# Performance work log

Hardware: AMD Instinct MI355X
Metric: run time of the kernel (lower is better)

Reference implementation:

```python
import jax, jax.numpy as jnp
import numpy as np

QLEN, BSZ, DM, NH, DH, FF = 1024, 4, 512, 8, 64, 2048
EPS = 1e-5


def layer_norm(x, g, b):
    mu = x.mean(-1, keepdims=True)
    var = ((x - mu) ** 2).mean(-1, keepdims=True)
    return (x - mu) / jnp.sqrt(var + EPS) * g + b


def rel_pos_emb(qlen, klen, d_model, bsz):
    # XLNet-style 'bi' relative positional encoding: positions klen .. -qlen+1
    freq = jnp.arange(0, d_model, 2, dtype=jnp.float32)
    inv_freq = 1.0 / (10000.0 ** (freq / d_model))
    pos_seq = jnp.arange(klen, -qlen, -1, dtype=jnp.float32)  # [klen+qlen]
    sinusoid = pos_seq[:, None] * inv_freq[None, :]           # [klen+qlen, d/2]
    pe = jnp.concatenate([jnp.sin(sinusoid), jnp.cos(sinusoid)], -1)
    return jnp.broadcast_to(pe[:, None, :], (pe.shape[0], bsz, d_model))


def rel_shift(x, klen):
    # x: [q, p, b, n] with p = klen + qlen
    q, p, b, n = x.shape
    x = x.reshape(p, q, b, n)[1:]
    x = x.reshape(q, p - 1, b, n)[:, :klen]
    return x


def setup_inputs() -> dict:
    key = jax.random.key(0)
    ks = jax.random.split(key, 20)
    s = 0.02
    inp = {
        'src': jax.random.normal(ks[0], (QLEN, BSZ, DM), jnp.float32),
        'q_w': jax.random.normal(ks[1], (DM, NH, DH), jnp.float32) * s,
        'k_w': jax.random.normal(ks[2], (DM, NH, DH), jnp.float32) * s,
        'v_w': jax.random.normal(ks[3], (DM, NH, DH), jnp.float32) * s,
        'r_w': jax.random.normal(ks[4], (DM, NH, DH), jnp.float32) * s,
        'o_w': jax.random.normal(ks[5], (DM, NH, DH), jnp.float32) * s,
        'r_w_bias': jax.random.normal(ks[6], (NH, DH), jnp.float32) * s,
        'r_r_bias': jax.random.normal(ks[7], (NH, DH), jnp.float32) * s,
        'w1': jax.random.normal(ks[8], (FF, DM), jnp.float32) * s,
        'b1': jnp.zeros((FF,), jnp.float32),
        'w2': jax.random.normal(ks[9], (DM, FF), jnp.float32) * s,
        'b2': jnp.zeros((DM,), jnp.float32),
        'g1': jnp.ones((DM,), jnp.float32), 'be1': jnp.zeros((DM,), jnp.float32),
        'g2': jnp.ones((DM,), jnp.float32), 'be2': jnp.zeros((DM,), jnp.float32),
        'gf': jnp.ones((DM,), jnp.float32), 'bf': jnp.zeros((DM,), jnp.float32),
        'src_mask': jnp.triu(jnp.ones((QLEN, QLEN), bool), k=1),
    }
    return inp


def reference(src, q_w, k_w, v_w, r_w, o_w, r_w_bias, r_r_bias,
              w1, b1, w2, b2, g1, be1, g2, be2, gf, bf, src_mask):
    qlen, bsz, dm = src.shape
    klen = qlen  # mems=None
    scale = 1.0 / (DH ** 0.5)
    pos_emb = rel_pos_emb(qlen, klen, dm, bsz)  # [klen+qlen, b, d]
    mask = src_mask.astype(src.dtype)

    # --- RelativeMultiheadAttention (single weight-shared encoder layer) ---
    cat = src  # no memory
    q_head = jnp.einsum('ibh,hnd->ibnd', src, q_w)
    k_head = jnp.einsum('ibh,hnd->ibnd', cat, k_w)
    v_head = jnp.einsum('ibh,hnd->ibnd', cat, v_w)
    k_pos = jnp.einsum('ibh,hnd->ibnd', pos_emb, r_w)

    ac = jnp.einsum('ibnd,jbnd->ijbn', q_head + r_w_bias, k_head)
    bd = jnp.einsum('ibnd,jbnd->ijbn', q_head + r_r_bias, k_pos)
    bd = rel_shift(bd, klen)

    score = (ac + bd) * scale - 1e30 * mask[:, :, None, None]
    prob = jax.nn.softmax(score, axis=1)
    attn_vec = jnp.einsum('ijbn,jbnd->ibnd', prob, v_head)
    attn_out = jnp.einsum('ibnd,hnd->ibh', attn_vec, o_w)

    x = layer_norm(src + attn_out, g1, be1)
    ffn = jax.nn.gelu(x @ w1.T + b1, approximate=False) @ w2.T + b2
    x = layer_norm(x + ffn, g2, be2)

    # final encoder norm
    out = layer_norm(x, gf, bf)
    return out
```

## Files before the change

kernel.cpp:

```cpp
#include <hip/hip_runtime.h>

#define QLEN 1024
#define BSZ  4
#define DM   512
#define NH   8
#define DH   64
#define FFD  2048

static constexpr float LN_EPS = 1e-5f;

typedef __attribute__((ext_vector_type(8))) short short8_t;
typedef __attribute__((ext_vector_type(4))) float f32x4;

__device__ __forceinline__ ushort f2b(float f) {
  uint u = __float_as_uint(f);
  return (ushort)((u + 0x7FFFu + ((u >> 16) & 1u)) >> 16);
}
__device__ __forceinline__ float b2f(ushort h) {
  return __uint_as_float(((uint)h) << 16);
}

__device__ __forceinline__ void cvt8_body(const float* in, ushort* out, int idx) {
  const float4 f0 = *reinterpret_cast<const float4*>(in + (size_t)idx * 8);
  const float4 f1 = *reinterpret_cast<const float4*>(in + (size_t)idx * 8 + 4);
  uint p0 = f2b(f0.x) | ((uint)f2b(f0.y) << 16);
  uint p1 = f2b(f0.z) | ((uint)f2b(f0.w) << 16);
  uint p2 = f2b(f1.x) | ((uint)f2b(f1.y) << 16);
  uint p3 = f2b(f1.z) | ((uint)f2b(f1.w) << 16);
  int4 st; st.x = (int)p0; st.y = (int)p1; st.z = (int)p2; st.w = (int)p3;
  *reinterpret_cast<int4*>(out + (size_t)idx * 8) = st;
}

__global__ __launch_bounds__(256) void prep_kernel(
    const float* __restrict__ src, const float* __restrict__ o_w,
    const float* __restrict__ w1, const float* __restrict__ w2,
    const float* __restrict__ qw, const float* __restrict__ kw,
    const float* __restrict__ vw, const float* __restrict__ rw,
    ushort* __restrict__ peb, ushort* __restrict__ srcb,
    ushort* __restrict__ owb, ushort* __restrict__ w1b,
    ushort* __restrict__ w2b, ushort* __restrict__ qkvw,
    ushort* __restrict__ rwT) {
  __shared__ float tile[32][33];
  const int bid = blockIdx.x, t = threadIdx.x;
  if (bid < 2048) {
    const int idx = bid * 256 + t;
    const int r = idx >> 9, f = idx & 511, f0 = f & 255;
    float invf = __expf(-(float)f0 * (9.210340371976184f / 256.0f));
    float arg  = (float)r * invf;
    peb[idx] = f2b((f < 256) ? __sinf(arg) : __cosf(arg));
  } else if (bid < 3072) {
    cvt8_body(src, srcb, (bid - 2048) * 256 + t);
  } else if (bid < 3200) {
    cvt8_body(o_w, owb, (bid - 3072) * 256 + t);
  } else if (bid < 3712) {
    cvt8_body(w1, w1b, (bid - 3200) * 256 + t);
  } else if (bid < 4224) {
    cvt8_body(w2, w2b, (bid - 3712) * 256 + t);
  } else {
    const int e = bid - 4224;
    const int z = e >> 8, rem = e & 255, bx = rem & 15, by = rem >> 4;
    const float* in = (z == 0) ? qw : (z == 1) ? kw : (z == 2) ? vw : rw;
    const int nd0 = bx * 32, h0 = by * 32;
    const int tx = t & 31, ty = t >> 5;
#pragma unroll
    for (int k = 0; k < 4; ++k)
      tile[ty + 8 * k][tx] = in[(size_t)(h0 + ty + 8 * k) * 512 + nd0 + tx];
    __syncthreads();
    ushort* out = (z < 3) ? (qkvw + (size_t)z * 512 * 512) : rwT;
#pragma unroll
    for (int k = 0; k < 4; ++k)
      out[(size_t)(nd0 + ty + 8 * k) * 512 + h0 + tx] = f2b(tile[tx][ty + 8 * k]);
  }
}

template <int EPI>
__global__ __launch_bounds__(256) void gemm_bf16(
    const ushort* __restrict__ A, const ushort* __restrict__ B,
    const float* __restrict__ bias, void* __restrict__ Cout,
    int M, int N, int K) {
  __shared__ ushort As[64 * 40];
  __shared__ ushort Bs[128 * 40];
  const int t = threadIdx.x;
  const int w = t >> 6, l = t & 63;
  const int lc = l & 15, lq = l >> 4;
  const int bm = blockIdx.y * 64, bn = blockIdx.x * 128;
  const int wr = (w >> 1) * 32, wc = (w & 1) * 64;
  const int sr = t >> 2, sk = (t & 3) * 8;

  f32x4 acc[2][4];
#pragma unroll
  for (int i = 0; i < 2; ++i)
#pragma unroll
    for (int j = 0; j < 4; ++j) acc[i][j] = (f32x4){0.f, 0.f, 0.f, 0.f};

  int4 a_v = *reinterpret_cast<const int4*>(A + (size_t)(bm + sr) * K + sk);
  int4 b0v = *reinterpret_cast<const int4*>(B + (size_t)(bn + sr) * K + sk);
  int4 b1v = *reinterpret_cast<const int4*>(B + (size_t)(bn + 64 + sr) * K + sk);

  for (int k0 = 0; k0 < K; k0 += 32) {
    *reinterpret_cast<int4*>(As + sr * 40 + sk) = a_v;
    *reinterpret_cast<int4*>(Bs + sr * 40 + sk) = b0v;
    *reinterpret_cast<int4*>(Bs + (64 + sr) * 40 + sk) = b1v;
    __syncthreads();
    if (k0 + 32 < K) {
      a_v = *reinterpret_cast<const int4*>(A + (size_t)(bm + sr) * K + k0 + 32 + sk);
      b0v = *reinterpret_cast<const int4*>(B + (size_t)(bn + sr) * K + k0 + 32 + sk);
      b1v = *reinterpret_cast<const int4*>(B + (size_t)(bn + 64 + sr) * K + k0 + 32 + sk);
    }
    short8_t af[2], bf[4];
#pragma unroll
    for (int mf = 0; mf < 2; ++mf)
      af[mf] = *reinterpret_cast<const short8_t*>(As + (wr + mf * 16 + lc) * 40 + lq * 8);
#pragma unroll
    for (int nf = 0; nf < 4; ++nf)
      bf[nf] = *reinterpret_cast<const short8_t*>(Bs + (wc + nf * 16 + lc) * 40 + lq * 8);
#pragma unroll
    for (int mf = 0; mf < 2; ++mf)
#pragma unroll
      for (int nf = 0; nf < 4; ++nf)
        acc[mf][nf] = __builtin_amdgcn_mfma_f32_16x16x32_bf16(af[mf], bf[nf], acc[mf][nf], 0, 0, 0);
    __syncthreads();
  }

#pragma unroll
  for (int mf = 0; mf < 2; ++mf)
#pragma unroll
    for (int nf = 0; nf < 4; ++nf) {
      const int col = bn + wc + nf * 16 + lc;
#pragma unroll
      for (int reg = 0; reg < 4; ++reg) {
        const int row = bm + wr + mf * 16 + lq * 4 + reg;
        float v = acc[mf][nf][reg];
        if (EPI == 2 || EPI == 3) v += bias[col];
        if (EPI == 2) v = 0.5f * v * (1.0f + erff(v * 0.70710678118654752f));
        if (EPI == 0 || EPI == 2)
          ((ushort*)Cout)[(size_t)row * N + col] = f2b(v);
        else
          ((float*)Cout)[(size_t)row * N + col] = v;
      }
    }
}

template <int EPI>
__global__ __launch_bounds__(256) void gemm128(
    const ushort* __restrict__ A, const ushort* __restrict__ B,
    const float* __restrict__ bias, void* __restrict__ Cout,
    int M, int N, int K) {
  __shared__ ushort As[128 * 40];
  __shared__ ushort Bs[128 * 40];
  const int t = threadIdx.x;
  const int w = t >> 6, l = t & 63;
  const int lc = l & 15, lq = l >> 4;
  const int bm = blockIdx.y * 128, bn = blockIdx.x * 128;
  const int wr = (w >> 1) * 64, wc = (w & 1) * 64;
  const int sr = t >> 2, sk = (t & 3) * 8;

  f32x4 acc[4][4];
#pragma unroll
  for (int i = 0; i < 4; ++i)
#pragma unroll
    for (int j = 0; j < 4; ++j) acc[i][j] = (f32x4){0.f, 0.f, 0.f, 0.f};

  int4 a0v = *reinterpret_cast<const int4*>(A + (size_t)(bm + sr) * K + sk);
  int4 a1v = *reinterpret_cast<const int4*>(A + (size_t)(bm + 64 + sr) * K + sk);
  int4 b0v = *reinterpret_cast<const int4*>(B + (size_t)(bn + sr) * K + sk);
  int4 b1v = *reinterpret_cast<const int4*>(B + (size_t)(bn + 64 + sr) * K + sk);

  for (int k0 = 0; k0 < K; k0 += 32) {
    *reinterpret_cast<int4*>(As + sr * 40 + sk) = a0v;
    *reinterpret_cast<int4*>(As + (64 + sr) * 40 + sk) = a1v;
    *reinterpret_cast<int4*>(Bs + sr * 40 + sk) = b0v;
    *reinterpret_cast<int4*>(Bs + (64 + sr) * 40 + sk) = b1v;
    __syncthreads();
    if (k0 + 32 < K) {
      a0v = *reinterpret_cast<const int4*>(A + (size_t)(bm + sr) * K + k0 + 32 + sk);
      a1v = *reinterpret_cast<const int4*>(A + (size_t)(bm + 64 + sr) * K + k0 + 32 + sk);
      b0v = *reinterpret_cast<const int4*>(B + (size_t)(bn + sr) * K + k0 + 32 + sk);
      b1v = *reinterpret_cast<const int4*>(B + (size_t)(bn + 64 + sr) * K + k0 + 32 + sk);
    }
    short8_t af[4], bf[4];
#pragma unroll
    for (int mf = 0; mf < 4; ++mf)
      af[mf] = *reinterpret_cast<const short8_t*>(As + (wr + mf * 16 + lc) * 40 + lq * 8);
#pragma unroll
    for (int nf = 0; nf < 4; ++nf)
      bf[nf] = *reinterpret_cast<const short8_t*>(Bs + (wc + nf * 16 + lc) * 40 + lq * 8);
#pragma unroll
    for (int mf = 0; mf < 4; ++mf)
#pragma unroll
      for (int nf = 0; nf < 4; ++nf)
        acc[mf][nf] = __builtin_amdgcn_mfma_f32_16x16x32_bf16(af[mf], bf[nf], acc[mf][nf], 0, 0, 0);
    __syncthreads();
  }

#pragma unroll
  for (int mf = 0; mf < 4; ++mf)
#pragma unroll
    for (int nf = 0; nf < 4; ++nf) {
      const int col = bn + wc + nf * 16 + lc;
#pragma unroll
      for (int reg = 0; reg < 4; ++reg) {
        const int row = bm + wr + mf * 16 + lq * 4 + reg;
        float v = acc[mf][nf][reg];
        if (EPI == 2 || EPI == 3) v += bias[col];
        if (EPI == 2) v = 0.5f * v * (1.0f + erff(v * 0.70710678118654752f));
        if (EPI == 0 || EPI == 2)
          ((ushort*)Cout)[(size_t)row * N + col] = f2b(v);
        else
          ((float*)Cout)[(size_t)row * N + col] = v;
      }
    }
}

__global__ __launch_bounds__(256) void gemm_split(
    const ushort* __restrict__ A, const ushort* __restrict__ B,
    float* __restrict__ Cout, int M, int N, int K, int halfK) {
  __shared__ ushort As[64 * 40];
  __shared__ ushort Bs[128 * 40];
  const int t = threadIdx.x;
  const int w = t >> 6, l = t & 63;
  const int lc = l & 15, lq = l >> 4;
  const int bm = blockIdx.y * 64, bn = blockIdx.x * 128;
  const int wr = (w >> 1) * 32, wc = (w & 1) * 64;
  const int sr = t >> 2, sk = (t & 3) * 8;
  const int kbeg = blockIdx.z * halfK, kend = kbeg + halfK;
  float* C = Cout + (size_t)blockIdx.z * M * N;

  f32x4 acc[2][4];
#pragma unroll
  for (int i = 0; i < 2; ++i)
#pragma unroll
    for (int j = 0; j < 4; ++j) acc[i][j] = (f32x4){0.f, 0.f, 0.f, 0.f};

  int4 a_v = *reinterpret_cast<const int4*>(A + (size_t)(bm + sr) * K + kbeg + sk);
  int4 b0v = *reinterpret_cast<const int4*>(B + (size_t)(bn + sr) * K + kbeg + sk);
  int4 b1v = *reinterpret_cast<const int4*>(B + (size_t)(bn + 64 + sr) * K + kbeg + sk);

  for (int k0 = kbeg; k0 < kend; k0 += 32) {
    *reinterpret_cast<int4*>(As + sr * 40 + sk) = a_v;
    *reinterpret_cast<int4*>(Bs + sr * 40 + sk) = b0v;
    *reinterpret_cast<int4*>(Bs + (64 + sr) * 40 + sk) = b1v;
    __syncthreads();
    if (k0 + 32 < kend) {
      a_v = *reinterpret_cast<const int4*>(A + (size_t)(bm + sr) * K + k0 + 32 + sk);
      b0v = *reinterpret_cast<const int4*>(B + (size_t)(bn + sr) * K + k0 + 32 + sk);
      b1v = *reinterpret_cast<const int4*>(B + (size_t)(bn + 64 + sr) * K + k0 + 32 + sk);
    }
    short8_t af[2], bf[4];
#pragma unroll
    for (int mf = 0; mf < 2; ++mf)
      af[mf] = *reinterpret_cast<const short8_t*>(As + (wr + mf * 16 + lc) * 40 + lq * 8);
#pragma unroll
    for (int nf = 0; nf < 4; ++nf)
      bf[nf] = *reinterpret_cast<const short8_t*>(Bs + (wc + nf * 16 + lc) * 40 + lq * 8);
#pragma unroll
    for (int mf = 0; mf < 2; ++mf)
#pragma unroll
      for (int nf = 0; nf < 4; ++nf)
        acc[mf][nf] = __builtin_amdgcn_mfma_f32_16x16x32_bf16(af[mf], bf[nf], acc[mf][nf], 0, 0, 0);
    __syncthreads();
  }

#pragma unroll
  for (int mf = 0; mf < 2; ++mf)
#pragma unroll
    for (int nf = 0; nf < 4; ++nf) {
      const int col = bn + wc + nf * 16 + lc;
#pragma unroll
      for (int reg = 0; reg < 4; ++reg) {
        const int row = bm + wr + mf * 16 + lq * 4 + reg;
        C[(size_t)row * N + col] = acc[mf][nf][reg];
      }
    }
}

__global__ __launch_bounds__(256) void repack_kernel(
    const ushort* __restrict__ qkv, const float* __restrict__ rwb,
    const float* __restrict__ rrb, ushort* __restrict__ qaF,
    ushort* __restrict__ qbF, ushort* __restrict__ kF, ushort* __restrict__ vF) {
  __shared__ ushort st[32][72];
  const int t = threadIdx.x, l = t & 63, lc = l & 15, lq = l >> 4;
  const int tile = blockIdx.x, head = blockIdx.y, role = blockIdx.z;
  const int b = head >> 3, n = head & 7;
  const int s0 = tile * 32;
  const int sec = (role == 0) ? 0 : (role == 1) ? 512 : 1024;
  {
    const int s = t >> 3, d8 = (t & 7) * 8;
    int4 rd = *reinterpret_cast<const int4*>(
        qkv + (size_t)((s0 + s) * 4 + b) * 1536 + sec + n * 64 + d8);
    *reinterpret_cast<int4*>(&st[s][d8]) = rd;
  }
  __syncthreads();
  if (role == 0) {
    const int f = t >> 6, sub = f >> 1, kc = f & 1;
    const int row = sub * 16 + lc, k = kc * 32 + lq * 8;
    short8_t qv = *reinterpret_cast<const short8_t*>(&st[row][k]);
    const float4 w0 = *reinterpret_cast<const float4*>(rwb + n * 64 + k);
    const float4 w1 = *reinterpret_cast<const float4*>(rwb + n * 64 + k + 4);
    const float4 u0 = *reinterpret_cast<const float4*>(rrb + n * 64 + k);
    const float4 u1 = *reinterpret_cast<const float4*>(rrb + n * 64 + k + 4);
    const float wv[8] = {w0.x, w0.y, w0.z, w0.w, w1.x, w1.y, w1.z, w1.w};
    const float uv[8] = {u0.x, u0.y, u0.z, u0.w, u1.x, u1.y, u1.z, u1.w};
    short8_t a_, b_;
#pragma unroll
    for (int e = 0; e < 8; ++e) {
      float q = b2f((ushort)qv[e]);
      a_[e] = (short)f2b(q + wv[e]);
      b_[e] = (short)f2b(q + uv[e]);
    }
    const size_t o = ((size_t)((head * 64 + tile * 2 + sub) * 2 + kc)) * 512 + l * 8;
    *reinterpret_cast<short8_t*>(qaF + o) = a_;
    *reinterpret_cast<short8_t*>(qbF + o) = b_;
  } else if (role == 1) {
    const int f = t >> 6, sub = f >> 1, kc = f & 1;
    const int row = sub * 16 + lc, k = kc * 32 + lq * 8;
    short8_t kv = *reinterpret_cast<const short8_t*>(&st[row][k]);
    const size_t o = ((size_t)((head * 64 + tile * 2 + sub) * 2 + kc)) * 512 + l * 8;
    *reinterpret_cast<short8_t*>(kF + o) = kv;
  } else {
    const int nf = t >> 6;
    short8_t vv;
#pragma unroll
    for (int e = 0; e < 8; ++e) vv[e] = (short)st[lq * 8 + e][nf * 16 + lc];
    const size_t o = ((size_t)((head * 32 + tile) * 4 + nf)) * 512 + l * 8;
    *reinterpret_cast<short8_t*>(vF + o) = vv;
  }
}

__global__ __launch_bounds__(128) void kprelF_kernel(
    const ushort* __restrict__ kprel, ushort* __restrict__ kprelF) {
  const int t = threadIdx.x, l = t & 63, lc = l & 15, lq = l >> 4;
  const int kc = t >> 6;
  const int m = blockIdx.x, n = blockIdx.y;
  const int rho = m * 16 - 31 + lc;
  short8_t v;
  if (rho >= 0 && rho < 1024)
    v = *reinterpret_cast<const short8_t*>(kprel + (size_t)rho * 512 + n * 64 + kc * 32 + lq * 8);
  else
#pragma unroll
    for (int e = 0; e < 8; ++e) v[e] = 0;
  const size_t o = ((size_t)((n * 66 + m) * 2 + kc)) * 512 + l * 8;
  *reinterpret_cast<short8_t*>(kprelF + o) = v;
}

__global__ __launch_bounds__(256, 4) void attn_mfma(
    const ushort* __restrict__ qaF, const ushort* __restrict__ qbF,
    const ushort* __restrict__ kF, const ushort* __restrict__ kpF,
    const ushort* __restrict__ vF, ushort* __restrict__ av) {
  __shared__ __align__(16) char smemU[22016];

  const int t = threadIdx.x, w = t >> 6, l = t & 63;
  const int lid = blockIdx.y * 32 + blockIdx.x;
  const int head = (lid & 7) * 4 + ((lid >> 3) & 3);
  const int pr   = lid >> 5;
  const int b = head >> 3, n = head & 7;
  const int lc = l & 15, lq = l >> 4;

  float*  gw = reinterpret_cast<float*>(smemU) + w * (16 * 66);
  ushort* pw = reinterpret_cast<ushort*>(smemU + 16896) + w * (16 * 40);

  for (int ph = 0; ph < 2; ++ph) {
    const int it = ph ? 63 - pr : pr;
    const int i0 = it * 16;
    __syncthreads();

    short8_t qa[2], qb[2];
    {
      const size_t qo = ((size_t)(head * 64 + it) * 2) * 512 + l * 8;
      qa[0] = *reinterpret_cast<const short8_t*>(qaF + qo);
      qa[1] = *reinterpret_cast<const short8_t*>(qaF + qo + 512);
      qb[0] = *reinterpret_cast<const short8_t*>(qbF + qo);
      qb[1] = *reinterpret_cast<const short8_t*>(qbF + qo + 512);
    }

    float m_run[4], l_lane[4];
    f32x4 oacc[4];
#pragma unroll
    for (int reg = 0; reg < 4; ++reg) { m_run[reg] = -1e30f; l_lane[reg] = 0.f; }
#pragma unroll
    for (int nf = 0; nf < 4; ++nf) oacc[nf] = (f32x4){0.f, 0.f, 0.f, 0.f};

    const int nj = it / 2 + 1;

    for (int jt = w; jt < nj; jt += 4) {
      const int j0 = jt * 32;
      const int D = i0 - j0;

      f32x4 sacc[2];
#pragma unroll
      for (int nf = 0; nf < 2; ++nf) sacc[nf] = (f32x4){0.f, 0.f, 0.f, 0.f};
#pragma unroll
      for (int kc = 0; kc < 2; ++kc)
#pragma unroll
        for (int nf = 0; nf < 2; ++nf) {
          short8_t kf = *reinterpret_cast<const short8_t*>(
              kF + ((size_t)((head * 64 + (j0 >> 4) + nf) * 2 + kc)) * 512 + l * 8);
          sacc[nf] = __builtin_amdgcn_mfma_f32_16x16x32_bf16(qa[kc], kf, sacc[nf], 0, 0, 0);
        }

      f32x4 gacc[3];
#pragma unroll
      for (int nf = 0; nf < 3; ++nf) gacc[nf] = (f32x4){0.f, 0.f, 0.f, 0.f};
#pragma unroll
      for (int kc = 0; kc < 2; ++kc)
#pragma unroll
        for (int nf = 0; nf < 3; ++nf) {
          short8_t pf = *reinterpret_cast<const short8_t*>(
              kpF + ((size_t)((n * 66 + (D >> 4) + nf) * 2 + kc)) * 512 + l * 8);
          gacc[nf] = __builtin_amdgcn_mfma_f32_16x16x32_bf16(qb[kc], pf, gacc[nf], 0, 0, 0);
        }

#pragma unroll
      for (int nf = 0; nf < 3; ++nf)
#pragma unroll
        for (int reg = 0; reg < 4; ++reg)
          gw[(lq * 4 + reg) * 66 + nf * 16 + lc] = gacc[nf][reg];

      float s0v[4], s1v[4];
#pragma unroll
      for (int reg = 0; reg < 4; ++reg) {
        const int r = lq * 4 + reg;
        const int c0 = lc, c1 = 16 + lc;
        float s0 = (sacc[0][reg] + gw[r * 66 + (r - c0 + 31)]) * 0.125f;
        float s1 = (sacc[1][reg] + gw[r * 66 + (r - c1 + 31)]) * 0.125f;
        if (D < 32) {
          if (c0 > D + r) s0 = -1e30f;
          if (c1 > D + r) s1 = -1e30f;
        }
        s0v[reg] = s0; s1v[reg] = s1;
      }
      bool ok = true;
#pragma unroll
      for (int reg = 0; reg < 4; ++reg)
        ok &= (fmaxf(s0v[reg], s1v[reg]) <= m_run[reg] + 8.0f);
      if (__all(ok ? 1 : 0)) {
#pragma unroll
        for (int reg = 0; reg < 4; ++reg) {
          const int r = lq * 4 + reg;
          const float p0 = __expf(s0v[reg] - m_run[reg]);
          const float p1 = __expf(s1v[reg] - m_run[reg]);
          l_lane[reg] += p0 + p1;
          pw[r * 40 + lc] = f2b(p0);
          pw[r * 40 + 16 + lc] = f2b(p1);
        }
      } else {
#pragma unroll
        for (int reg = 0; reg < 4; ++reg) {
          const int r = lq * 4 + reg;
          float tm = fmaxf(s0v[reg], s1v[reg]);
          tm = fmaxf(tm, __shfl_xor(tm, 1));
          tm = fmaxf(tm, __shfl_xor(tm, 2));
          tm = fmaxf(tm, __shfl_xor(tm, 4));
          tm = fmaxf(tm, __shfl_xor(tm, 8));
          const float mn = fmaxf(m_run[reg], tm);
          const float corr = __expf(m_run[reg] - mn);
          const float p0 = __expf(s0v[reg] - mn), p1 = __expf(s1v[reg] - mn);
          l_lane[reg] = l_lane[reg] * corr + (p0 + p1);
          m_run[reg] = mn;
#pragma unroll
          for (int nf = 0; nf < 4; ++nf) oacc[nf][reg] *= corr;
          pw[r * 40 + lc] = f2b(p0);
          pw[r * 40 + 16 + lc] = f2b(p1);
        }
      }

      short8_t pa = *reinterpret_cast<const short8_t*>(pw + lc * 40 + lq * 8);
#pragma unroll
      for (int nf = 0; nf < 4; ++nf) {
        short8_t vf = *reinterpret_cast<const short8_t*>(
            vF + ((size_t)((head * 32 + jt) * 4 + nf)) * 512 + l * 8);
        oacc[nf] = __builtin_amdgcn_mfma_f32_16x16x32_bf16(pa, vf, oacc[nf], 0, 0, 0);
      }
    }

    float l_run[4];
#pragma unroll
    for (int reg = 0; reg < 4; ++reg) {
      float v = l_lane[reg];
      v += __shfl_xor(v, 1);
      v += __shfl_xor(v, 2);
      v += __shfl_xor(v, 4);
      v += __shfl_xor(v, 8);
      l_run[reg] = v;
    }

    __syncthreads();
    float* obuf = reinterpret_cast<float*>(smemU);
    float* mlb  = reinterpret_cast<float*>(smemU + 4352);

    if (lc == 0) {
#pragma unroll
      for (int reg = 0; reg < 4; ++reg) {
        const int r = lq * 4 + reg;
        mlb[(w * 16 + r) * 2 + 0] = m_run[reg];
        mlb[(w * 16 + r) * 2 + 1] = l_run[reg];
      }
    }
    for (int i = t; i < 16 * 68; i += 256) obuf[i] = 0.f;
    __syncthreads();

    float scl[4];
#pragma unroll
    for (int reg = 0; reg < 4; ++reg) {
      const int r = lq * 4 + reg;
      const float m0 = mlb[r * 2], m1 = mlb[(16 + r) * 2],
                  m2 = mlb[(32 + r) * 2], m3 = mlb[(48 + r) * 2];
      const float ms = fmaxf(fmaxf(m0, m1), fmaxf(m2, m3));
      scl[reg] = __expf(mlb[(w * 16 + r) * 2] - ms);
    }
#pragma unroll
    for (int ww = 0; ww < 4; ++ww) {
      if (w == ww) {
#pragma unroll
        for (int nf = 0; nf < 4; ++nf)
#pragma unroll
          for (int reg = 0; reg < 4; ++reg) {
            const int r = lq * 4 + reg;
            obuf[r * 68 + nf * 16 + lc] += scl[reg] * oacc[nf][reg];
          }
      }
      __syncthreads();
    }

    {
      const int r = t >> 4, d0 = (t & 15) * 4;
      const float m0 = mlb[r * 2], m1 = mlb[(16 + r) * 2],
                  m2 = mlb[(32 + r) * 2], m3 = mlb[(48 + r) * 2];
      const float ms = fmaxf(fmaxf(m0, m1), fmaxf(m2, m3));
      const float ls = mlb[r * 2 + 1] * __expf(m0 - ms) + mlb[(16 + r) * 2 + 1] * __expf(m1 - ms) +
                       mlb[(32 + r) * 2 + 1] * __expf(m2 - ms) + mlb[(48 + r) * 2 + 1] * __expf(m3 - ms);
      const float inv = 1.f / ls;
      uint pk0 = (uint)f2b(obuf[r * 68 + d0] * inv) | ((uint)f2b(obuf[r * 68 + d0 + 1] * inv) << 16);
      uint pk1 = (uint)f2b(obuf[r * 68 + d0 + 2] * inv) | ((uint)f2b(obuf[r * 68 + d0 + 3] * inv) << 16);
      int2 st2; st2.x = (int)pk0; st2.y = (int)pk1;
      const int tok = (i0 + r) * 4 + b;
      *reinterpret_cast<int2*>(av + (size_t)tok * 512 + n * 64 + d0) = st2;
    }
  }
}

__device__ __forceinline__ float blk_sum(float v, volatile float* sb) {
  v += __shfl_xor(v, 1);  v += __shfl_xor(v, 2);  v += __shfl_xor(v, 4);
  v += __shfl_xor(v, 8);  v += __shfl_xor(v, 16); v += __shfl_xor(v, 32);
  const int t = threadIdx.x;
  if ((t & 63) == 0) sb[t >> 6] = v;
  __syncthreads();
  v = sb[0] + sb[1] + sb[2] + sb[3];
  __syncthreads();
  return v;
}

__global__ __launch_bounds__(256) void ln_res_kernel(
    const float* __restrict__ aoa, const float* __restrict__ aob,
    const float* __restrict__ res,
    const float* __restrict__ g, const float* __restrict__ be,
    float* __restrict__ out, ushort* __restrict__ outb) {
  __shared__ float sb[4];
  const int row = blockIdx.x, t = threadIdx.x;
  const size_t base = (size_t)row * DM;
  const float x0 = aoa[base + t] + aob[base + t] + res[base + t];
  const float x1 = aoa[base + t + 256] + aob[base + t + 256] + res[base + t + 256];
  const float mu = blk_sum(x0 + x1, sb) * (1.f / DM);
  const float d0 = x0 - mu, d1 = x1 - mu;
  const float var = blk_sum(d0 * d0 + d1 * d1, sb) * (1.f / DM);
  const float inv = rsqrtf(var + LN_EPS);
  const float z0 = d0 * inv * g[t] + be[t];
  const float z1 = d1 * inv * g[t + 256] + be[t + 256];
  out[base + t] = z0;
  out[base + t + 256] = z1;
  outb[base + t] = f2b(z0);
  outb[base + t + 256] = f2b(z1);
}

__global__ __launch_bounds__(256) void ln_final_kernel(
    const float* __restrict__ ya, const float* __restrict__ yb,
    const float* __restrict__ b2, const float* __restrict__ xres,
    const float* __restrict__ g2, const float* __restrict__ be2,
    const float* __restrict__ gf, const float* __restrict__ bf,
    float* __restrict__ out) {
  __shared__ float sb[4];
  const int row = blockIdx.x, t = threadIdx.x;
  const size_t base = (size_t)row * DM;
  const float x0 = ya[base + t] + yb[base + t] + b2[t] + xres[base + t];
  const float x1 = ya[base + t + 256] + yb[base + t + 256] + b2[t + 256] + xres[base + t + 256];
  const float mu = blk_sum(x0 + x1, sb) * (1.f / DM);
  const float d0 = x0 - mu, d1 = x1 - mu;
  const float var = blk_sum(d0 * d0 + d1 * d1, sb) * (1.f / DM);
  const float inv = rsqrtf(var + LN_EPS);
  const float z0 = d0 * inv * g2[t] + be2[t];
  const float z1 = d1 * inv * g2[t + 256] + be2[t + 256];
  const float mu2 = blk_sum(z0 + z1, sb) * (1.f / DM);
  const float e0 = z0 - mu2, e1 = z1 - mu2;
  const float var2 = blk_sum(e0 * e0 + e1 * e1, sb) * (1.f / DM);
  const float inv2 = rsqrtf(var2 + LN_EPS);
  out[base + t]       = e0 * inv2 * gf[t] + bf[t];
  out[base + t + 256] = e1 * inv2 * gf[t + 256] + bf[t + 256];
}

extern "C" void kernel_launch(void* const* d_in, const int* in_sizes, int n_in,
                              void* d_out, int out_size, void* d_ws, size_t ws_size,
                              hipStream_t stream) {
  const float* src = (const float*)d_in[0];
  const float* q_w = (const float*)d_in[1];
  const float* k_w = (const float*)d_in[2];
  const float* v_w = (const float*)d_in[3];
  const float* r_w = (const float*)d_in[4];
  const float* o_w = (const float*)d_in[5];
  const float* rwb = (const float*)d_in[6];
  const float* rrb = (const float*)d_in[7];
  const float* w1  = (const float*)d_in[8];
  const float* b1  = (const float*)d_in[9];
  const float* w2  = (const float*)d_in[10];
  const float* b2  = (const float*)d_in[11];
  const float* g1  = (const float*)d_in[12];
  const float* be1 = (const float*)d_in[13];
  const float* g2  = (const float*)d_in[14];
  const float* be2 = (const float*)d_in[15];
  const float* gf  = (const float*)d_in[16];
  const float* bf  = (const float*)d_in[17];

  char* ws = (char*)d_ws;
  const size_t KB = 1024, MB = 1024 * 1024;
  ushort* srcb   = (ushort*)(ws);
  ushort* qkvw   = (ushort*)(ws + 4 * MB);
  ushort* rwT    = (ushort*)(ws + 5 * MB + 512 * KB);
  ushort* owb    = (ushort*)(ws + 6 * MB);
  ushort* w1b    = (ushort*)(ws + 6 * MB + 512 * KB);
  ushort* w2b    = (ushort*)(ws + 8 * MB + 512 * KB);
  ushort* peb    = (ushort*)(ws + 10 * MB + 512 * KB);
  ushort* qkv    = (ushort*)(ws + 11 * MB + 512 * KB);
  ushort* kprel  = (ushort*)(ws + 23 * MB + 512 * KB);
  ushort* qaF    = (ushort*)(ws + 24 * MB + 512 * KB);
  ushort* qbF    = (ushort*)(ws + 28 * MB + 512 * KB);
  ushort* kF     = (ushort*)(ws + 32 * MB + 512 * KB);
  ushort* vF     = (ushort*)(ws + 36 * MB + 512 * KB);
  ushort* kprelF = (ushort*)(ws + 40 * MB + 512 * KB);
  ushort* av     = (ushort*)(ws + 42 * MB);
  float*  aoP    = (float*) (ws + 24 * MB + 512 * KB);
  float*  x1     = (float*) (ws + 46 * MB);
  ushort* x1b    = (ushort*)(ws + 42 * MB);
  ushort* h      = (ushort*)(ws + 11 * MB + 512 * KB);
  float*  y2P    = (float*) (ws + 27 * MB + 512 * KB);
  float*  outp   = (float*)d_out;

  prep_kernel<<<dim3(5248), 256, 0, stream>>>(src, o_w, w1, w2, q_w, k_w, v_w, r_w,
                                              peb, srcb, owb, w1b, w2b, qkvw, rwT);

  gemm128<0><<<dim3(12, 32), 256, 0, stream>>>(srcb, qkvw, nullptr, qkv, 4096, 1536, 512);
  gemm_bf16<0><<<dim3(4, 16), 256, 0, stream>>>(peb, rwT, nullptr, kprel, 1024, 512, 512);

  repack_kernel<<<dim3(32, 32, 3), 256, 0, stream>>>(qkv, rwb, rrb, qaF, qbF, kF, vF);
  kprelF_kernel<<<dim3(66, 8), 128, 0, stream>>>(kprel, kprelF);

  attn_mfma<<<dim3(32, 32), 256, 0, stream>>>(qaF, qbF, kF, kprelF, vF, av);

  gemm_split<<<dim3(4, 64, 2), 256, 0, stream>>>(av, owb, aoP, 4096, 512, 512, 256);
  ln_res_kernel<<<dim3(4096), 256, 0, stream>>>(aoP, aoP + 2097152, src, g1, be1, x1, x1b);

  gemm128<2><<<dim3(16, 32), 256, 0, stream>>>(x1b, w1b, b1, h, 4096, 2048, 512);
  gemm_split<<<dim3(4, 64, 2), 256, 0, stream>>>(h, w2b, y2P, 4096, 512, 2048, 1024);

  ln_final_kernel<<<dim3(4096), 256, 0, stream>>>(y2P, y2P + 2097152, b2, x1, g2, be2, gf, bf, outp);
}
```

Measured before the change: 144.8 us.

## Merge QKV and positional GEMMs, fold kprelF into repack, shuffle rel-shift via bpermute

Runs the QKV projection and the positional-key projection in a single launch with a shared 128x128 tile body. The kprelF relayout now runs as extra blocks of the repack kernel, which removes one launch. In attention, the relative-shift gather of the positional scores uses ds_bpermute lane shuffles instead of a per-wave shared-memory staging buffer, which shrinks shared memory from about 22KB to 5KB per block. The goal is fewer launches, less LDS traffic and higher occupancy, at the cost of more complex lane-index logic.

```diff
diff --git a/kernel.cpp b/kernel.cpp
--- a/kernel.cpp
+++ b/kernel.cpp
@@ -73,49 +73,47 @@
   }
 }
 
-template <int EPI>
-__global__ __launch_bounds__(256) void gemm_bf16(
-    const ushort* __restrict__ A, const ushort* __restrict__ B,
-    const float* __restrict__ bias, void* __restrict__ Cout,
-    int M, int N, int K) {
-  __shared__ ushort As[64 * 40];
-  __shared__ ushort Bs[128 * 40];
-  const int t = threadIdx.x;
+__device__ __forceinline__ void gemm128_body(
+    const ushort* A, const ushort* B, ushort* C,
+    int N, int K, int bm, int bn, int t,
+    ushort* As, ushort* Bs) {
   const int w = t >> 6, l = t & 63;
   const int lc = l & 15, lq = l >> 4;
-  const int bm = blockIdx.y * 64, bn = blockIdx.x * 128;
-  const int wr = (w >> 1) * 32, wc = (w & 1) * 64;
+  const int wr = (w >> 1) * 64, wc = (w & 1) * 64;
   const int sr = t >> 2, sk = (t & 3) * 8;
 
-  f32x4 acc[2][4];
-#pragma unroll
-  for (int i = 0; i < 2; ++i)
+  f32x4 acc[4][4];
+#pragma unroll
+  for (int i = 0; i < 4; ++i)
 #pragma unroll
     for (int j = 0; j < 4; ++j) acc[i][j] = (f32x4){0.f, 0.f, 0.f, 0.f};
 
-  int4 a_v = *reinterpret_cast<const int4*>(A + (size_t)(bm + sr) * K + sk);
+  int4 a0v = *reinterpret_cast<const int4*>(A + (size_t)(bm + sr) * K + sk);
+  int4 a1v = *reinterpret_cast<const int4*>(A + (size_t)(bm + 64 + sr) * K + sk);
   int4 b0v = *reinterpret_cast<const int4*>(B + (size_t)(bn + sr) * K + sk);
   int4 b1v = *reinterpret_cast<const int4*>(B + (size_t)(bn + 64 + sr) * K + sk);
 
   for (int k0 = 0; k0 < K; k0 += 32) {
-    *reinterpret_cast<int4*>(As + sr * 40 + sk) = a_v;
+    *reinterpret_cast<int4*>(As + sr * 40 + sk) = a0v;
+    *reinterpret_cast<int4*>(As + (64 + sr) * 40 + sk) = a1v;
     *reinterpret_cast<int4*>(Bs + sr * 40 + sk) = b0v;
     *reinterpret_cast<int4*>(Bs + (64 + sr) * 40 + sk) = b1v;
     __syncthreads();
     if (k0 + 32 < K) {
-      a_v = *reinterpret_cast<const int4*>(A + (size_t)(bm + sr) * K + k0 + 32 + sk);
+      a0v = *reinterpret_cast<const int4*>(A + (size_t)(bm + sr) * K + k0 + 32 + sk);
+      a1v = *reinterpret_cast<const int4*>(A + (size_t)(bm + 64 + sr) * K + k0 + 32 + sk);
       b0v = *reinterpret_cast<const int4*>(B + (size_t)(bn + sr) * K + k0 + 32 + sk);
       b1v = *reinterpret_cast<const int4*>(B + (size_t)(bn + 64 + sr) * K + k0 + 32 + sk);
     }
-    short8_t af[2], bf[4];
-#pragma unroll
-    for (int mf = 0; mf < 2; ++mf)
+    short8_t af[4], bf[4];
+#pragma unroll
+    for (int mf = 0; mf < 4; ++mf)
       af[mf] = *reinterpret_cast<const short8_t*>(As + (wr + mf * 16 + lc) * 40 + lq * 8);
 #pragma unroll
     for (int nf = 0; nf < 4; ++nf)
       bf[nf] = *reinterpret_cast<const short8_t*>(Bs + (wc + nf * 16 + lc) * 40 + lq * 8);
 #pragma unroll
-    for (int mf = 0; mf < 2; ++mf)
+    for (int mf = 0; mf < 4; ++mf)
 #pragma unroll
       for (int nf = 0; nf < 4; ++nf)
         acc[mf][nf] = __builtin_amdgcn_mfma_f32_16x16x32_bf16(af[mf], bf[nf], acc[mf][nf], 0, 0, 0);
@@ -123,28 +121,38 @@
   }
 
 #pragma unroll
-  for (int mf = 0; mf < 2; ++mf)
+  for (int mf = 0; mf < 4; ++mf)
 #pragma unroll
     for (int nf = 0; nf < 4; ++nf) {
       const int col = bn + wc + nf * 16 + lc;
 #pragma unroll
       for (int reg = 0; reg < 4; ++reg) {
         const int row = bm + wr + mf * 16 + lq * 4 + reg;
-        float v = acc[mf][nf][reg];
-        if (EPI == 2 || EPI == 3) v += bias[col];
-        if (EPI == 2) v = 0.5f * v * (1.0f + erff(v * 0.70710678118654752f));
-        if (EPI == 0 || EPI == 2)
-          ((ushort*)Cout)[(size_t)row * N + col] = f2b(v);
-        else
-          ((float*)Cout)[(size_t)row * N + col] = v;
-      }
-    }
-}
-
-template <int EPI>
-__global__ __launch_bounds__(256) void gemm128(
+        C[(size_t)row * N + col] = f2b(acc[mf][nf][reg]);
+      }
+    }
+}
+
+__global__ __launch_bounds__(256) void gemm128_dual(
+    const ushort* __restrict__ srcb, const ushort* __restrict__ qkvw,
+    const ushort* __restrict__ peb, const ushort* __restrict__ rwT,
+    ushort* __restrict__ qkv, ushort* __restrict__ kprel) {
+  __shared__ ushort As[128 * 40];
+  __shared__ ushort Bs[128 * 40];
+  const int bid = blockIdx.x, t = threadIdx.x;
+  if (bid < 384) {
+    const int bx = bid % 12, by = bid / 12;
+    gemm128_body(srcb, qkvw, qkv, 1536, 512, by * 128, bx * 128, t, As, Bs);
+  } else {
+    const int e = bid - 384;
+    const int bx = e & 3, by = e >> 2;
+    gemm128_body(peb, rwT, kprel, 512, 512, by * 128, bx * 128, t, As, Bs);
+  }
+}
+
+__global__ __launch_bounds__(256) void gemm128_gelu(
     const ushort* __restrict__ A, const ushort* __restrict__ B,
-    const float* __restrict__ bias, void* __restrict__ Cout,
+    const float* __restrict__ bias, ushort* __restrict__ Cout,
     int M, int N, int K) {
   __shared__ ushort As[128 * 40];
   __shared__ ushort Bs[128 * 40];
@@ -201,13 +209,9 @@
 #pragma unroll
       for (int reg = 0; reg < 4; ++reg) {
         const int row = bm + wr + mf * 16 + lq * 4 + reg;
-        float v = acc[mf][nf][reg];
-        if (EPI == 2 || EPI == 3) v += bias[col];
-        if (EPI == 2) v = 0.5f * v * (1.0f + erff(v * 0.70710678118654752f));
-        if (EPI == 0 || EPI == 2)
-          ((ushort*)Cout)[(size_t)row * N + col] = f2b(v);
-        else
-          ((float*)Cout)[(size_t)row * N + col] = v;
+        float v = acc[mf][nf][reg] + bias[col];
+        v = 0.5f * v * (1.0f + erff(v * 0.70710678118654752f));
+        Cout[(size_t)row * N + col] = f2b(v);
       }
     }
 }
@@ -276,11 +280,33 @@
 
 __global__ __launch_bounds__(256) void repack_kernel(
     const ushort* __restrict__ qkv, const float* __restrict__ rwb,
-    const float* __restrict__ rrb, ushort* __restrict__ qaF,
-    ushort* __restrict__ qbF, ushort* __restrict__ kF, ushort* __restrict__ vF) {
+    const float* __restrict__ rrb, const ushort* __restrict__ kprel,
+    ushort* __restrict__ qaF, ushort* __restrict__ qbF,
+    ushort* __restrict__ kF, ushort* __restrict__ vF,
+    ushort* __restrict__ kprelF) {
   __shared__ ushort st[32][72];
-  const int t = threadIdx.x, l = t & 63, lc = l & 15, lq = l >> 4;
-  const int tile = blockIdx.x, head = blockIdx.y, role = blockIdx.z;
+  const int bid = blockIdx.x, t = threadIdx.x;
+  const int l = t & 63, lc = l & 15, lq = l >> 4;
+
+  if (bid >= 3072) {
+    if (t < 128) {
+      const int e = bid - 3072;
+      const int m = e % 66, n = e / 66;
+      const int kc = t >> 6;
+      const int rho = m * 16 - 31 + lc;
+      short8_t v;
+      if (rho >= 0 && rho < 1024)
+        v = *reinterpret_cast<const short8_t*>(kprel + (size_t)rho * 512 + n * 64 + kc * 32 + lq * 8);
+      else
+#pragma unroll
+        for (int e2 = 0; e2 < 8; ++e2) v[e2] = 0;
+      const size_t o = ((size_t)((n * 66 + m) * 2 + kc)) * 512 + l * 8;
+      *reinterpret_cast<short8_t*>(kprelF + o) = v;
+    }
+    return;
+  }
+
+  const int tile = bid & 31, head = (bid >> 5) & 31, role = bid >> 10;
   const int b = head >> 3, n = head & 7;
   const int s0 = tile * 32;
   const int sec = (role == 0) ? 0 : (role == 1) ? 512 : 1024;
@@ -327,27 +353,11 @@
   }
 }
 
-__global__ __launch_bounds__(128) void kprelF_kernel(
-    const ushort* __restrict__ kprel, ushort* __restrict__ kprelF) {
-  const int t = threadIdx.x, l = t & 63, lc = l & 15, lq = l >> 4;
-  const int kc = t >> 6;
-  const int m = blockIdx.x, n = blockIdx.y;
-  const int rho = m * 16 - 31 + lc;
-  short8_t v;
-  if (rho >= 0 && rho < 1024)
-    v = *reinterpret_cast<const short8_t*>(kprel + (size_t)rho * 512 + n * 64 + kc * 32 + lq * 8);
-  else
-#pragma unroll
-    for (int e = 0; e < 8; ++e) v[e] = 0;
-  const size_t o = ((size_t)((n * 66 + m) * 2 + kc)) * 512 + l * 8;
-  *reinterpret_cast<short8_t*>(kprelF + o) = v;
-}
-
 __global__ __launch_bounds__(256, 4) void attn_mfma(
     const ushort* __restrict__ qaF, const ushort* __restrict__ qbF,
     const ushort* __restrict__ kF, const ushort* __restrict__ kpF,
     const ushort* __restrict__ vF, ushort* __restrict__ av) {
-  __shared__ __align__(16) char smemU[22016];
+  __shared__ __align__(16) char smemU[5120];
 
   const int t = threadIdx.x, w = t >> 6, l = t & 63;
   const int lid = blockIdx.y * 32 + blockIdx.x;
@@ -356,8 +366,7 @@
   const int b = head >> 3, n = head & 7;
   const int lc = l & 15, lq = l >> 4;
 
-  float*  gw = reinterpret_cast<float*>(smemU) + w * (16 * 66);
-  ushort* pw = reinterpret_cast<ushort*>(smemU + 16896) + w * (16 * 40);
+  ushort* pw = reinterpret_cast<ushort*>(smemU) + w * (16 * 40);
 
   for (int ph = 0; ph < 2; ++ph) {
     const int it = ph ? 63 - pr : pr;
@@ -410,25 +419,26 @@
           gacc[nf] = __builtin_amdgcn_mfma_f32_16x16x32_bf16(qb[kc], pf, gacc[nf], 0, 0, 0);
         }
 
-#pragma unroll
-      for (int nf = 0; nf < 3; ++nf)
-#pragma unroll
-        for (int reg = 0; reg < 4; ++reg)
-          gw[(lq * 4 + reg) * 66 + nf * 16 + lc] = gacc[nf][reg];
-
       float s0v[4], s1v[4];
 #pragma unroll
-      for (int reg = 0; reg < 4; ++reg) {
-        const int r = lq * 4 + reg;
-        const int c0 = lc, c1 = 16 + lc;
-        float s0 = (sacc[0][reg] + gw[r * 66 + (r - c0 + 31)]) * 0.125f;
-        float s1 = (sacc[1][reg] + gw[r * 66 + (r - c1 + 31)]) * 0.125f;
+      for (int j = 0; j < 4; ++j) {
+        const int r = lq * 4 + j;
+        const int sl4 = ((((r + 15 - lc) & 15) | (lq << 4)) << 2);
+        const float g0 = __int_as_float(__builtin_amdgcn_ds_bpermute(sl4, __float_as_int(gacc[0][j])));
+        const float g1 = __int_as_float(__builtin_amdgcn_ds_bpermute(sl4, __float_as_int(gacc[1][j])));
+        const float g2 = __int_as_float(__builtin_amdgcn_ds_bpermute(sl4, __float_as_int(gacc[2][j])));
+        const bool sel = (r <= lc);
+        const float Gu0 = sel ? g1 : g2;
+        const float Gu1 = sel ? g0 : g1;
+        float s0 = (sacc[0][j] + Gu0) * 0.125f;
+        float s1 = (sacc[1][j] + Gu1) * 0.125f;
         if (D < 32) {
-          if (c0 > D + r) s0 = -1e30f;
-          if (c1 > D + r) s1 = -1e30f;
+          if (lc > D + r) s0 = -1e30f;
+          if (16 + lc > D + r) s1 = -1e30f;
         }
-        s0v[reg] = s0; s1v[reg] = s1;
-      }
+        s0v[j] = s0; s1v[j] = s1;
+      }
+
       bool ok = true;
 #pragma unroll
       for (int reg = 0; reg < 4; ++reg)
@@ -646,18 +656,16 @@
   prep_kernel<<<dim3(5248), 256, 0, stream>>>(src, o_w, w1, w2, q_w, k_w, v_w, r_w,
                                               peb, srcb, owb, w1b, w2b, qkvw, rwT);
 
-  gemm128<0><<<dim3(12, 32), 256, 0, stream>>>(srcb, qkvw, nullptr, qkv, 4096, 1536, 512);
-  gemm_bf16<0><<<dim3(4, 16), 256, 0, stream>>>(peb, rwT, nullptr, kprel, 1024, 512, 512);
-
-  repack_kernel<<<dim3(32, 32, 3), 256, 0, stream>>>(qkv, rwb, rrb, qaF, qbF, kF, vF);
-  kprelF_kernel<<<dim3(66, 8), 128, 0, stream>>>(kprel, kprelF);
+  gemm128_dual<<<dim3(416), 256, 0, stream>>>(srcb, qkvw, peb, rwT, qkv, kprel);
+
+  repack_kernel<<<dim3(3600), 256, 0, stream>>>(qkv, rwb, rrb, kprel, qaF, qbF, kF, vF, kprelF);
 
   attn_mfma<<<dim3(32, 32), 256, 0, stream>>>(qaF, qbF, kF, kprelF, vF, av);
 
   gemm_split<<<dim3(4, 64, 2), 256, 0, stream>>>(av, owb, aoP, 4096, 512, 512, 256);
   ln_res_kernel<<<dim3(4096), 256, 0, stream>>>(aoP, aoP + 2097152, src, g1, be1, x1, x1b);
 
-  gemm128<2><<<dim3(16, 32), 256, 0, stream>>>(x1b, w1b, b1, h, 4096, 2048, 512);
+  gemm128_gelu<<<dim3(16, 32), 256, 0, stream>>>(x1b, w1b, b1, h, 4096, 2048, 512);
   gemm_split<<<dim3(4, 64, 2), 256, 0, stream>>>(h, w2b, y2P, 4096, 512, 2048, 1024);
 
   ln_final_kernel<<<dim3(4096), 256, 0, stream>>>(y2P, y2P + 2097152, b2, x1, g2, be2, gf, bf, outp);
```

Measured after the change: 134.3 us, median of 2. 7.3% less time.
